# Kernel optimization log

Measured on AMD Instinct MI355X. Metric: run time of the kernel, lower is better.

The kernel has to match this reference:

```python
import jax, jax.numpy as jnp
import numpy as np

VGG_MEAN = jnp.array([0.485, 0.456, 0.406], jnp.float32).reshape(1, 3, 1, 1)
VGG_STD = jnp.array([0.229, 0.224, 0.225], jnp.float32).reshape(1, 3, 1, 1)
SCALE = 2


def _bicubic_matrix(n_in, n_out, a=-0.75):
    # torch F.interpolate(mode='bicubic', align_corners=True): src = i*(n_in-1)/(n_out-1), cubic a=-0.75
    i = np.arange(n_out)
    src = i * (n_in - 1) / (n_out - 1)
    f = np.floor(src).astype(np.int64)
    t = src - f

    def kern(x):
        x = np.abs(x)
        return np.where(x <= 1.0, (a + 2) * x**3 - (a + 3) * x**2 + 1.0,
                        np.where(x < 2.0, a * x**3 - 5 * a * x**2 + 8 * a * x - 4 * a, 0.0))

    M = np.zeros((n_out, n_in), np.float64)
    for off in (-1, 0, 1, 2):
        idx = np.clip(f + off, 0, n_in - 1)
        np.add.at(M, (i, idx), kern(t - off))
    return jnp.asarray(M, jnp.float32)


def _bicubic_up(x, scale):
    B, C, H, W = x.shape
    Mh = _bicubic_matrix(H, H * scale)
    Mw = _bicubic_matrix(W, W * scale)
    x = jnp.einsum('oh,bchw->bcow', Mh, x)
    return jnp.einsum('pw,bcow->bcop', Mw, x)


def _conv(x, w, b, pad):
    y = jax.lax.conv_general_dilated(x, w, (1, 1), ((pad, pad), (pad, pad)),
                                     dimension_numbers=('NCHW', 'OIHW', 'NCHW'))
    return y + b[None, :, None, None]


def _features(x, w1, b1, w2, b2, w3, b3, wm, bm):
    # VGG19 features[0:7] + BasicBlock(128->16, 1x1, LeakyReLU 0.2)
    x = jax.nn.relu(_conv(x, w1, b1, 1))
    x = jax.nn.relu(_conv(x, w2, b2, 1))
    x = jax.lax.reduce_window(x, -jnp.inf, jax.lax.max, (1, 1, 2, 2), (1, 1, 2, 2), 'VALID')
    x = jax.nn.relu(_conv(x, w3, b3, 1))
    x = jax.nn.leaky_relu(_conv(x, wm, bm, 0), 0.2)
    return x


def _patches(x):
    # im2col like F.unfold: output feature dim ordered (C, kh, kw), same as torch
    p = jax.lax.conv_general_dilated_patches(x, (3, 3), (1, 1), ((1, 1), (1, 1)))
    B, Ck, H, W = p.shape
    return p.reshape(B, Ck, H * W)


def _forward(query, key, w1, b1, w2, b2, w3, b3, wm, bm, flag_8k):
    q = (query - VGG_MEAN) / VGG_STD
    if not flag_8k:
        q = _bicubic_up(q, SCALE)
    q = _features(q, w1, b1, w2, b2, w3, b3, wm, bm)
    B, C, Hq, Wq = q.shape
    qp = _patches(q)                                      # [B, C*9, Lq]
    qp = qp / jnp.maximum(jnp.linalg.norm(qp, axis=1, keepdims=True), 1e-12)

    B2, C2, Hk, Wk = key.shape
    k = key.reshape(B2, C2, Hk // SCALE, SCALE, Wk // SCALE, SCALE).mean((3, 5))  # AvgPool2d(scale)
    k = (k - VGG_MEAN) / VGG_STD
    if not flag_8k:
        k = _bicubic_up(k, SCALE)
    k = _features(k, w1, b1, w2, b2, w3, b3, wm, bm)
    kp = jnp.transpose(_patches(k), (0, 2, 1))            # [B, Lk, C*9]
    kp = kp / jnp.maximum(jnp.linalg.norm(kp, axis=2, keepdims=True), 1e-12)

    y = jnp.einsum('bkc,bcq->bkq', kp, qp)                # [B, Lk, Lq] cosine similarities
    rel = jnp.max(y, axis=1).reshape(B, 1, Hq, Wq)
    idx = jnp.argmax(y, axis=1)
    return rel, idx


def setup_inputs():
    key0 = jax.random.key(0)
    ks = jax.random.split(key0, 6)
    return {
        'query': jax.random.uniform(ks[0], (1, 3, 120, 120), jnp.float32),
        'key': jax.random.uniform(ks[1], (1, 3, 240, 240), jnp.float32),
        'w1': jax.random.normal(ks[2], (64, 3, 3, 3), jnp.float32) * 0.05,
        'b1': jnp.zeros((64,), jnp.float32),
        'w2': jax.random.normal(ks[3], (64, 64, 3, 3), jnp.float32) * 0.05,
        'b2': jnp.zeros((64,), jnp.float32),
        'w3': jax.random.normal(ks[4], (128, 64, 3, 3), jnp.float32) * 0.05,
        'b3': jnp.zeros((128,), jnp.float32),
        'wm': jax.random.normal(ks[5], (16, 128, 1, 1), jnp.float32) * 0.05,
        'bm': jnp.zeros((16,), jnp.float32),
        'flag_8k': 0,
    }


def reference(query, key, w1, b1, w2, b2, w3, b3, wm, bm, flag_8k):
    return _forward(query, key, w1, b1, w2, b2, w3, b3, wm, bm, flag_8k)
```

## Files before the change

### kernel.cpp

```cpp
#include <hip/hip_runtime.h>
#include <math.h>

#define H0 120
#define W0 120
#define H1 240
#define W1 240
#define L  14400
#define FDIM 144
#define CPAD 160
#define LPAD 14464

#define KC     128
#define NCHT   113
#define NCHB   8
#define NGRAN  904
#define NLIST  32
#define MARGIN 6.5e-3f

typedef _Float16 half8 __attribute__((ext_vector_type(8)));
typedef float    f32x4 __attribute__((ext_vector_type(4)));

__device__ __forceinline__ double meanc(int c){ return c==0?0.485:(c==1?0.456:0.406); }
__device__ __forceinline__ double stdc (int c){ return c==0?0.229:(c==1?0.224:0.225); }

__global__ __launch_bounds__(256) void k_cvt_all(const float* __restrict__ w1, const float* __restrict__ b1,
                                                 const float* __restrict__ w2, const float* __restrict__ b2,
                                                 const float* __restrict__ w3, const float* __restrict__ b3,
                                                 const float* __restrict__ wm, const float* __restrict__ bm,
                                                 double* __restrict__ wd){
  int i = blockIdx.x*256 + threadIdx.x;
  if (i >= 114640) return;
  float v;
  if      (i < 1728)   v = w1[i];
  else if (i < 1792)   v = b1[i-1728];
  else if (i < 38656)  v = w2[i-1792];
  else if (i < 38720)  v = b2[i-38656];
  else if (i < 112448) v = w3[i-38720];
  else if (i < 112576) v = b3[i-112448];
  else if (i < 114624) v = wm[i-112576];
  else                 v = bm[i-114624];
  wd[i] = (double)v;
}

__global__ __launch_bounds__(256) void k_prep(const float* __restrict__ query,
                                              const float* __restrict__ key,
                                              float* __restrict__ nq){
  int i = blockIdx.x*256 + threadIdx.x;
  if (i >= 2*3*L) return;
  int b = i/(3*L); int r = i - b*3*L; int c = r / L; int p = r - c*L;
  double v;
  if (b==0){
    v = (double)query[c*L + p];
  } else {
    int y = p / W0, x = p - y*W0;
    const float* kk = key + (size_t)c*(H1*W1);
    int yy = 2*y, xx = 2*x;
    v = 0.25*((double)kk[yy*W1+xx] + (double)kk[yy*W1+xx+1]
            + (double)kk[(yy+1)*W1+xx] + (double)kk[(yy+1)*W1+xx+1]);
  }
  nq[i] = (float)((v - meanc(c)) / stdc(c));
}

__device__ __forceinline__ double cubw(double x){
  x = fabs(x);
  if (x <= 1.0)      return (1.25*x - 2.25)*x*x + 1.0;
  else if (x < 2.0)  return -0.75*(((x - 5.0)*x + 8.0)*x - 4.0);
  return 0.0;
}

__global__ __launch_bounds__(256) void k_bicubic(const float* __restrict__ nq,
                                                 float* __restrict__ up){
  int i = blockIdx.x*256 + threadIdx.x;
  if (i >= 2*3*H1*W1) return;
  int bc = i/(H1*W1); int r = i - bc*H1*W1; int oy = r/W1, ox = r - oy*W1;
  double sy = (double)oy * (double)(H0-1) / (double)(H1-1);
  double sx = (double)ox * (double)(W0-1) / (double)(W1-1);
  int fy = (int)floor(sy); double ty = sy - (double)fy;
  int fx = (int)floor(sx); double tx = sx - (double)fx;
  double wy[4], wx[4]; int iy[4], ix[4];
  #pragma unroll
  for (int o=0;o<4;++o){
    wy[o] = cubw(ty - (double)(o-1));
    wx[o] = cubw(tx - (double)(o-1));
    int yv = fy + o - 1; iy[o] = min(max(yv,0),H0-1);
    int xv = fx + o - 1; ix[o] = min(max(xv,0),W0-1);
  }
  const float* src = nq + (size_t)bc*(H0*W0);
  double acc = 0.0;
  #pragma unroll
  for (int j=0;j<4;++j){
    double colv = 0.0;
    #pragma unroll
    for (int a=0;a<4;++a) colv += wy[a]*(double)src[iy[a]*W0 + ix[j]];
    acc += wx[j]*colv;
  }
  up[i] = (float)acc;
}

template<int CIN, int CIC, int HW>
__global__ __launch_bounds__(256) void k_conv3x3(const float* __restrict__ in,
                                                 const double* __restrict__ w,
                                                 const double* __restrict__ bias,
                                                 float* __restrict__ out, int CO){
  constexpr int T = 30, TI = 32, TP = 36;
  constexpr int NT = HW / T;
  __shared__ __align__(16) float s_in[CIC][TI][TP];
  int tid = threadIdx.x;
  int tile = blockIdx.x; int trow = tile/NT;
  int ty0 = trow*T, tx0 = (tile - trow*NT)*T;
  int ocb = blockIdx.y*8; int b = blockIdx.z;
  const float* inb = in + (size_t)b*CIN*HW*HW;
  bool active = tid < 225;
  int tyy = (tid/15)*2, txx = (tid%15)*2;
  double acc[2][2][8];
  #pragma unroll
  for (int o=0;o<8;++o){
    double bv = bias[ocb+o];
    acc[0][0][o]=bv; acc[0][1][o]=bv; acc[1][0][o]=bv; acc[1][1][o]=bv;
  }
  for (int c0=0; c0<CIN; c0+=CIC){
    __syncthreads();
    for (int f4 = tid; f4 < CIC*256; f4 += 256){
      int ci = f4 >> 8; int rem = f4 & 255;
      int rr = rem >> 3; int c4 = rem & 7;
      int gy = ty0 + rr - 1, gx0 = tx0 + c4*4 - 1;
      float4 v = {0.f,0.f,0.f,0.f};
      if (gy >= 0 && gy < HW){
        const float* rowp = inb + (size_t)(c0+ci)*HW*HW + (size_t)gy*HW;
        float* vp = (float*)&v;
        #pragma unroll
        for (int e=0;e<4;++e){
          int gx = gx0 + e;
          if (gx >= 0 && gx < HW) vp[e] = rowp[gx];
        }
      }
      *(float4*)&s_in[ci][rr][c4*4] = v;
    }
    __syncthreads();
    if (active){
      for (int ci=0; ci<CIC; ++ci){
        double tap[4][4];
        #pragma unroll
        for (int rr=0;rr<4;++rr){
          float2 lo = *(const float2*)&s_in[ci][tyy+rr][txx];
          float2 hi = *(const float2*)&s_in[ci][tyy+rr][txx+2];
          tap[rr][0] = (double)lo.x; tap[rr][1] = (double)lo.y;
          tap[rr][2] = (double)hi.x; tap[rr][3] = (double)hi.y;
        }
        const double* wp = w + ((size_t)ocb*CIN + (c0+ci))*9;
        #pragma unroll
        for (int t=0;t<9;++t){
          const int ky = t/3, kx = t - ky*3;
          #pragma unroll
          for (int o=0;o<8;++o){
            double wv = wp[(size_t)o*CIN*9 + t];
            acc[0][0][o] += tap[ky+0][kx+0]*wv;
            acc[0][1][o] += tap[ky+0][kx+1]*wv;
            acc[1][0][o] += tap[ky+1][kx+0]*wv;
            acc[1][1][o] += tap[ky+1][kx+1]*wv;
          }
        }
      }
    }
  }
  if (active){
    #pragma unroll
    for (int py=0;py<2;++py)
      #pragma unroll
      for (int px=0;px<2;++px){
        int gy = ty0+tyy+py, gx = tx0+txx+px;
        float* op = out + ((size_t)(b*CO+ocb)*HW + gy)*HW + gx;
        #pragma unroll
        for (int o=0;o<8;++o){
          double v = acc[py][px][o];
          op[(size_t)o*HW*HW] = (float)(v>0.0 ? v : 0.0);
        }
      }
  }
}

__global__ __launch_bounds__(256) void k_maxpool(const float* __restrict__ in,
                                                 float* __restrict__ out){
  int i = blockIdx.x*256 + threadIdx.x;
  if (i >= 2*64*L) return;
  int bc = i / L; int p = i - bc*L; int y = p/W0, x = p - y*W0;
  const float* s = in + (size_t)bc*H1*W1;
  int yy = 2*y, xx = 2*x;
  out[i] = fmaxf(fmaxf(s[yy*W1+xx], s[yy*W1+xx+1]),
                 fmaxf(s[(yy+1)*W1+xx], s[(yy+1)*W1+xx+1]));
}

__global__ __launch_bounds__(256) void k_conv1x1(const float* __restrict__ in,
                                                 const double* __restrict__ wm,
                                                 const double* __restrict__ bm,
                                                 float* __restrict__ out){
  int i = blockIdx.x*256 + threadIdx.x;
  if (i >= 2*L) return;
  int b = i/L; int p = i - b*L;
  double a[16];
  #pragma unroll
  for (int o=0;o<16;++o) a[o] = bm[o];
  const float* src = in + (size_t)b*128*L + p;
  for (int ci=0; ci<128; ++ci){
    double v = (double)src[(size_t)ci*L];
    #pragma unroll
    for (int o=0;o<16;++o) a[o] += v * wm[o*128 + ci];
  }
  float* dst = out + (size_t)b*16*L + p;
  #pragma unroll
  for (int o=0;o<16;++o){ double v=a[o]; dst[(size_t)o*L] = (float)(v>0.0 ? v : 0.2*v); }
}

__global__ __launch_bounds__(256) void k_patches(const float* __restrict__ fm,
                                                 _Float16* __restrict__ Tq16,
                                                 _Float16* __restrict__ Tk16,
                                                 float* __restrict__ Tq32,
                                                 float* __restrict__ Tk32){
  __shared__ float s[16][4][120];
  __shared__ double rns[64];
  int b  = blockIdx.y;
  int bx = blockIdx.x;
  bool pad = (bx == 225);
  if (pad && b == 0) return;
  int tid = threadIdx.x;
  int pix0 = bx*64;
  int y0 = pad ? 119 : (pix0/120);
  int ybase = y0 - 1;
  const float* src = fm + (size_t)b*16*L;
  for (int e = tid; e < 16*4*120; e += 256){
    int c = e/480; int r = (e/120)&3; int x = e%120;
    int gy = ybase + r;
    s[c][r][x] = (gy>=0 && gy<H0) ? src[c*L + gy*W0 + x] : 0.f;
  }
  __syncthreads();
  if (tid < 64){
    int p = pad ? (L-1) : (pix0 + tid);
    int y = p/W0, x = p - y*W0;
    double ss = 0.0;
    for (int c=0;c<16;++c){
      #pragma unroll
      for (int dy=0;dy<3;++dy){
        int r = y + dy - 1 - ybase;
        #pragma unroll
        for (int dx=0;dx<3;++dx){
          int gx = x + dx - 1;
          double v = (gx>=0 && gx<W0) ? (double)s[c][r][gx] : 0.0;
          ss += v*v;
        }
      }
    }
    rns[tid] = 1.0 / fmax(sqrt(ss), 1e-12);
  }
  __syncthreads();
  _Float16* T16 = (b==0) ? Tq16 : Tk16;
  float*    T32 = (b==0) ? Tq32 : Tk32;
  for (int e = tid; e < 64*CPAD; e += 256){
    int row = e/CPAD, col = e - row*CPAD;
    int p = pad ? (L-1) : (pix0 + row);
    int outrow = pad ? (L + row) : p;
    float f = 0.f;
    if (col < FDIM){
      int c = col/9; int rem = col - c*9; int dy = rem/3; int dx = rem - dy*3;
      int y = p/W0, x = p - y*W0;
      int r = y + dy - 1 - ybase;
      int gx = x + dx - 1;
      float v = (gx>=0 && gx<W0) ? s[c][r][gx] : 0.f;
      f = (float)((double)v * rns[row]);
    }
    T32[(size_t)outrow*CPAD + col] = f;
    T16[(size_t)outrow*CPAD + col] = (_Float16)f;
  }
}

__global__ __launch_bounds__(256) void k_simh(const _Float16* __restrict__ Tq,
                                              const _Float16* __restrict__ Tk,
                                              _Float16* __restrict__ cmaxh){
  __shared__ __align__(16) _Float16 skT[40*512];
  int tid = threadIdx.x;
  int wid = tid >> 6, lane = tid & 63;
  int wk = wid & 1, wq = wid >> 1;
  int q0 = blockIdx.x * 96;
  int cg = lane >> 4;
  int qb = q0 + wq*48 + (lane & 15);
  half8 fB[3][5];
  #pragma unroll
  for (int bf=0; bf<3; ++bf)
    #pragma unroll
    for (int ks=0; ks<5; ++ks)
      fB[bf][ks] = *(const half8*)(Tq + (size_t)(qb + bf*16)*CPAD + ks*32 + cg*8);
  int ch0 = blockIdx.y * NCHB;
  for (int cc=0; cc<NCHB; ++cc){
    int chunk = ch0 + cc;
    if (chunk >= NCHT) break;
    int kbase = chunk * KC;
    __syncthreads();
    #pragma unroll
    for (int it=0; it<10; ++it){
      int b1 = wid*10 + it;
      int kg = b1 / 5, ks = b1 % 5;
      const _Float16* g = Tk + (size_t)(kbase + kg*16 + (lane&15))*CPAD + ks*32 + cg*8;
      __builtin_amdgcn_global_load_lds((const __attribute__((address_space(1))) void*)g,
                                       (__attribute__((address_space(3))) void*)(skT + b1*512),
                                       16, 0, 0);
    }
    __syncthreads();
    f32x4 acc[4][3];
    #pragma unroll
    for (int kf=0;kf<4;++kf)
      #pragma unroll
      for (int bf=0;bf<3;++bf)
        acc[kf][bf] = (f32x4){0.f,0.f,0.f,0.f};
    #pragma unroll
    for (int ks=0; ks<5; ++ks){
      #pragma unroll
      for (int kf=0; kf<4; ++kf){
        half8 av = *(const half8*)(skT + ((size_t)((wk*4+kf)*5 + ks))*512 + lane*8);
        #pragma unroll
        for (int bf=0; bf<3; ++bf)
          acc[kf][bf] = __builtin_amdgcn_mfma_f32_16x16x32_f16(av, fB[bf][ks], acc[kf][bf], 0, 0, 0);
      }
    }
    #pragma unroll
    for (int kf=0; kf<4; ++kf){
      int gran = chunk*8 + wk*4 + kf;
      #pragma unroll
      for (int bf=0; bf<3; ++bf){
        f32x4 a = acc[kf][bf];
        float m = fmaxf(fmaxf(a.x, a.y), fmaxf(a.z, a.w));
        m = fmaxf(m, __shfl_xor(m, 16));
        m = fmaxf(m, __shfl_xor(m, 32));
        float mb = m * (m >= 0.f ? 1.0009765625f : 0.9990234375f);
        if (lane < 16)
          cmaxh[(size_t)gran*L + q0 + wq*48 + bf*16 + lane] = (_Float16)mb;
      }
    }
  }
}

__global__ __launch_bounds__(256) void k_flag(const _Float16* __restrict__ cmaxh,
                                              unsigned short* __restrict__ list,
                                              int* __restrict__ nf,
                                              float* __restrict__ thrv){
  int q    = blockIdx.x*4 + (threadIdx.x >> 6);
  int lane = threadIdx.x & 63;
  if (q >= L) return;
  float v[15];
  #pragma unroll
  for (int j=0;j<15;++j){
    int g = j*64 + lane;
    v[j] = (g < NGRAN) ? (float)cmaxh[(size_t)g*L + q] : -1e30f;
  }
  float m = -1e30f;
  #pragma unroll
  for (int j=0;j<15;++j) m = fmaxf(m, v[j]);
  #pragma unroll
  for (int d=32; d>=1; d>>=1) m = fmaxf(m, __shfl_xor(m, d));
  float thr = m - MARGIN;
  unsigned short* lst = list + (size_t)q*NLIST;
  int base = 0;
  #pragma unroll
  for (int j=0;j<15;++j){
    bool f = v[j] >= thr;
    unsigned long long mask = __ballot(f);
    if (f){
      int pos = base + __popcll(mask & ((1ull<<lane)-1ull));
      if (pos < NLIST) lst[pos] = (unsigned short)(j*64 + lane);
    }
    base += __popcll(mask);
  }
  if (lane == 0){ nf[q] = base; thrv[q] = thr; }
}

__global__ __launch_bounds__(64) void k_rescore3(const float* __restrict__ Tq32,
                                                 const float* __restrict__ Tk32,
                                                 const unsigned short* __restrict__ list,
                                                 const int* __restrict__ nf,
                                                 const float* __restrict__ thrv,
                                                 const _Float16* __restrict__ cmaxh,
                                                 float* __restrict__ out){
  int q = blockIdx.x, lane = threadIdx.x;
  int slot = lane & 15, quarter = lane >> 4;
  const float* qp = Tq32 + (size_t)q*CPAD + quarter*36;
  double q64[36];
  #pragma unroll
  for (int c=0;c<36;++c) q64[c] = (double)qp[c];
  int n = nf[q];
  float thr = thrv[q];
  double best = -1e300; int bi = 0x7fffffff;

  auto proc = [&](int g){
    int key = g*16 + slot;
    const float* kr = Tk32 + (size_t)key*CPAD + quarter*36;
    double s = 0.0;
    #pragma unroll
    for (int c=0;c<36;++c) s += q64[c]*(double)kr[c];
    s += __shfl_xor(s, 16);
    s += __shfl_xor(s, 32);
    if (key < L && s > best){ best = s; bi = key; }
  };

  if (n <= NLIST){
    const unsigned short* lst = list + (size_t)q*NLIST;
    for (int it=0; it<n; ++it) proc(lst[it]);
  } else {
    for (int g=0; g<NGRAN; ++g)
      if ((float)cmaxh[(size_t)g*L + q] >= thr) proc(g);
  }
  #pragma unroll
  for (int d=1; d<16; d<<=1){
    double v2 = __shfl_xor(best, d);
    int    i2 = __shfl_xor(bi, d);
    if (v2 > best || (v2 == best && i2 < bi)){ best = v2; bi = i2; }
  }
  if (lane == 0){
    out[q]     = (float)best;
    out[L + q] = (float)bi;
  }
}

extern "C" void kernel_launch(void* const* d_in, const int* in_sizes, int n_in,
                              void* d_out, int out_size, void* d_ws, size_t ws_size,
                              hipStream_t stream){
  const float* query = (const float*)d_in[0];
  const float* key   = (const float*)d_in[1];
  const float* w1 = (const float*)d_in[2];
  const float* b1 = (const float*)d_in[3];
  const float* w2 = (const float*)d_in[4];
  const float* b2 = (const float*)d_in[5];
  const float* w3 = (const float*)d_in[6];
  const float* b3 = (const float*)d_in[7];
  const float* wm = (const float*)d_in[8];
  const float* bm = (const float*)d_in[9];
  float* out = (float*)d_out;

  double* wd = (double*)d_ws;
  double* wd1 = wd;
  double* bd1 = wd + 1728;
  double* wd2 = wd + 1792;
  double* bd2 = wd + 38656;
  double* wd3 = wd + 38720;
  double* bd3 = wd + 112448;
  double* wdm = wd + 112576;
  double* bdm = wd + 114624;
  float* fbase = (float*)d_ws + 230400;
  float* nq = fbase;
  float* up = nq + 86400;
  float* A  = up + 345600;
  float* Bf = A  + 7372800;
  float* C  = A;
  float* D  = A + 1843200;
  float* FM = Bf + 7372800 - 460800;
  _Float16* Tq16 = (_Float16*)A;
  _Float16* Tk16 = (_Float16*)(A + 1152000);
  float*    Tq32 = A + 2309120;
  float*    Tk32 = Tq32 + 2304000;
  _Float16* cmaxh = (_Float16*)(A + 6927360);
  unsigned short* list = (unsigned short*)(A + 13436160);
  int*   nfl  = (int*)(A + 13666560);
  float* thrv = A + 13680960;

  k_cvt_all<<<(114640+255)/256, 256, 0, stream>>>(w1,b1,w2,b2,w3,b3,wm,bm, wd);

  k_prep   <<<(2*3*L + 255)/256, 256, 0, stream>>>(query, key, nq);
  k_bicubic<<<(2*3*H1*W1 + 255)/256, 256, 0, stream>>>(nq, up);
  k_conv3x3<3,3,240><<<dim3(64,8,2), 256, 0, stream>>>(up, wd1, bd1, A, 64);
  k_conv3x3<64,8,240><<<dim3(64,8,2), 256, 0, stream>>>(A, wd2, bd2, Bf, 64);
  k_maxpool<<<(2*64*L + 255)/256, 256, 0, stream>>>(Bf, C);
  k_conv3x3<64,8,120><<<dim3(16,16,2), 256, 0, stream>>>(C, wd3, bd3, D, 128);
  k_conv1x1<<<(2*L + 255)/256, 256, 0, stream>>>(D, wdm, bdm, FM);
  k_patches<<<dim3(226,2), 256, 0, stream>>>(FM, Tq16, Tk16, Tq32, Tk32);
  k_simh   <<<dim3(150, 15), 256, 0, stream>>>(Tq16, Tk16, cmaxh);
  k_flag   <<<(L + 3)/4, 256, 0, stream>>>(cmaxh, list, nfl, thrv);
  k_rescore3<<<L, 64, 0, stream>>>(Tq32, Tk32, list, nfl, thrv, cmaxh, out);
}
```

Before: 642.2 us.

## Double-buffer conv3x3 input tiles with register prefetch and fast interior loads

Restructures the direct 3x3 convolution so that the next channel chunk is loaded from global memory into registers while the current chunk is computed from shared memory. The data is then written into a second shared buffer, which removes one barrier per chunk. Interior tiles use unconditional float4 loads, skipping the per-element bounds checks. The channel chunk size drops from 8 to 4 to keep shared memory and registers in check, at the cost of more loop iterations and barriers.

```diff
diff --git a/kernel.cpp b/kernel.cpp
--- a/kernel.cpp
+++ b/kernel.cpp
@@ -104,50 +104,79 @@
                                                  float* __restrict__ out, int CO){
   constexpr int T = 30, TI = 32, TP = 36;
   constexpr int NT = HW / T;
-  __shared__ __align__(16) float s_in[CIC][TI][TP];
+  constexpr int NCH = CIN / CIC;
+  __shared__ __align__(16) float s_in[2][CIC][TI][TP];
   int tid = threadIdx.x;
-  int tile = blockIdx.x; int trow = tile/NT;
-  int ty0 = trow*T, tx0 = (tile - trow*NT)*T;
+  int tile = blockIdx.x; int trow = tile/NT; int tcol = tile - trow*NT;
+  int ty0 = trow*T, tx0 = tcol*T;
   int ocb = blockIdx.y*8; int b = blockIdx.z;
   const float* inb = in + (size_t)b*CIN*HW*HW;
   bool active = tid < 225;
   int tyy = (tid/15)*2, txx = (tid%15)*2;
+  int srr = tid >> 3, sc4 = tid & 7;
+  int sgy = ty0 + srr - 1, sgx0 = tx0 + sc4*4 - 1;
+  bool interior = (trow >= 1) && (trow <= NT-2) && (tcol >= 1) && (tcol <= NT-2);
+
   double acc[2][2][8];
   #pragma unroll
   for (int o=0;o<8;++o){
     double bv = bias[ocb+o];
     acc[0][0][o]=bv; acc[0][1][o]=bv; acc[1][0][o]=bv; acc[1][1][o]=bv;
   }
-  for (int c0=0; c0<CIN; c0+=CIC){
-    __syncthreads();
-    for (int f4 = tid; f4 < CIC*256; f4 += 256){
-      int ci = f4 >> 8; int rem = f4 & 255;
-      int rr = rem >> 3; int c4 = rem & 7;
-      int gy = ty0 + rr - 1, gx0 = tx0 + c4*4 - 1;
-      float4 v = {0.f,0.f,0.f,0.f};
-      if (gy >= 0 && gy < HW){
-        const float* rowp = inb + (size_t)(c0+ci)*HW*HW + (size_t)gy*HW;
-        float* vp = (float*)&v;
-        #pragma unroll
-        for (int e=0;e<4;++e){
-          int gx = gx0 + e;
-          if (gx >= 0 && gx < HW) vp[e] = rowp[gx];
+
+  float4 regs[CIC];
+  auto gload = [&](int c0){
+    if (interior){
+      #pragma unroll
+      for (int j=0;j<CIC;++j)
+        regs[j] = *(const float4*)(inb + (size_t)(c0+j)*HW*HW + (size_t)sgy*HW + sgx0);
+    } else {
+      bool colsok = (sgx0 >= 0) && (sgx0 + 3 < HW);
+      bool rowok  = (sgy >= 0) && (sgy < HW);
+      #pragma unroll
+      for (int j=0;j<CIC;++j){
+        float4 v = {0.f,0.f,0.f,0.f};
+        if (rowok){
+          const float* rowp = inb + (size_t)(c0+j)*HW*HW + (size_t)sgy*HW;
+          if (colsok){
+            v = *(const float4*)(rowp + sgx0);
+          } else {
+            float* vp = (float*)&v;
+            #pragma unroll
+            for (int e=0;e<4;++e){
+              int gx = sgx0 + e;
+              if (gx >= 0 && gx < HW) vp[e] = rowp[gx];
+            }
+          }
         }
+        regs[j] = v;
       }
-      *(float4*)&s_in[ci][rr][c4*4] = v;
-    }
-    __syncthreads();
+    }
+  };
+  auto swrite = [&](int buf){
+    #pragma unroll
+    for (int j=0;j<CIC;++j)
+      *(float4*)&s_in[buf][j][srr][sc4*4] = regs[j];
+  };
+
+  gload(0);
+  swrite(0);
+  __syncthreads();
+  for (int k=0; k<NCH; ++k){
+    int cur = k & 1;
+    if (k+1 < NCH) gload((k+1)*CIC);
     if (active){
+      #pragma unroll
       for (int ci=0; ci<CIC; ++ci){
         double tap[4][4];
         #pragma unroll
         for (int rr=0;rr<4;++rr){
-          float2 lo = *(const float2*)&s_in[ci][tyy+rr][txx];
-          float2 hi = *(const float2*)&s_in[ci][tyy+rr][txx+2];
+          float2 lo = *(const float2*)&s_in[cur][ci][tyy+rr][txx];
+          float2 hi = *(const float2*)&s_in[cur][ci][tyy+rr][txx+2];
           tap[rr][0] = (double)lo.x; tap[rr][1] = (double)lo.y;
           tap[rr][2] = (double)hi.x; tap[rr][3] = (double)hi.y;
         }
-        const double* wp = w + ((size_t)ocb*CIN + (c0+ci))*9;
+        const double* wp = w + ((size_t)ocb*CIN + (k*CIC+ci))*9;
         #pragma unroll
         for (int t=0;t<9;++t){
           const int ky = t/3, kx = t - ky*3;
@@ -162,7 +191,12 @@
         }
       }
     }
-  }
+    if (k+1 < NCH){
+      swrite(cur ^ 1);
+      __syncthreads();
+    }
+  }
+
   if (active){
     #pragma unroll
     for (int py=0;py<2;++py)
@@ -463,10 +497,10 @@
 
   k_prep   <<<(2*3*L + 255)/256, 256, 0, stream>>>(query, key, nq);
   k_bicubic<<<(2*3*H1*W1 + 255)/256, 256, 0, stream>>>(nq, up);
-  k_conv3x3<3,3,240><<<dim3(64,8,2), 256, 0, stream>>>(up, wd1, bd1, A, 64);
-  k_conv3x3<64,8,240><<<dim3(64,8,2), 256, 0, stream>>>(A, wd2, bd2, Bf, 64);
+  k_conv3x3<3,3,240> <<<dim3(64,8,2), 256, 0, stream>>>(up, wd1, bd1, A, 64);
+  k_conv3x3<64,4,240><<<dim3(64,8,2), 256, 0, stream>>>(A, wd2, bd2, Bf, 64);
   k_maxpool<<<(2*64*L + 255)/256, 256, 0, stream>>>(Bf, C);
-  k_conv3x3<64,8,120><<<dim3(16,16,2), 256, 0, stream>>>(C, wd3, bd3, D, 128);
+  k_conv3x3<64,4,120><<<dim3(16,16,2), 256, 0, stream>>>(C, wd3, bd3, D, 128);
   k_conv1x1<<<(2*L + 255)/256, 256, 0, stream>>>(D, wdm, bdm, FM);
   k_patches<<<dim3(226,2), 256, 0, stream>>>(FM, Tq16, Tk16, Tq32, Tk32);
   k_simh   <<<dim3(150, 15), 256, 0, stream>>>(Tq16, Tk16, cmaxh);
```

New measurement: 659.7 us. 1.03x slower.
